# Optimization experiments

Hardware: AMD Instinct MI355X
Metric: run time of the kernel (lower is better)

The kernel has to match this reference:

```python
import jax, jax.numpy as jnp
import numpy as np

K = 3
K2 = K * K
EPS = 1e-5


def conv2d(x, w, stride=1, pad=1):
    return jax.lax.conv_general_dilated(
        x, w, (stride, stride), [(pad, pad), (pad, pad)],
        dimension_numbers=("NCHW", "OIHW", "NCHW"))


def bilinear_sample(x, py, px):
    """x: [B,C,H,W]; py,px: [B,Ho,Wo,K2] float sample coords.
    Zero padding outside bounds (torchvision deform_conv2d semantics).
    Returns [B,C,Ho,Wo,K2]."""
    B, C, H, W = x.shape
    Ho, Wo = py.shape[1], py.shape[2]
    y0 = jnp.floor(py)
    x0 = jnp.floor(px)
    wy1 = py - y0
    wx1 = px - x0
    x_flat = x.reshape(B, C, H * W)

    def gather(yi, xi):
        valid = (yi >= 0) & (yi < H) & (xi >= 0) & (xi < W)
        yc = jnp.clip(yi, 0, H - 1).astype(jnp.int32)
        xc = jnp.clip(xi, 0, W - 1).astype(jnp.int32)
        idx = (yc * W + xc).reshape(B, 1, -1)          # [B,1,N]
        v = jnp.take_along_axis(x_flat, idx, axis=2)   # [B,C,N]
        return v * valid.reshape(B, 1, -1).astype(x.dtype)

    w00 = ((1 - wy1) * (1 - wx1)).reshape(B, 1, -1)
    w01 = ((1 - wy1) * wx1).reshape(B, 1, -1)
    w10 = (wy1 * (1 - wx1)).reshape(B, 1, -1)
    w11 = (wy1 * wx1).reshape(B, 1, -1)
    val = (w00 * gather(y0, x0) + w01 * gather(y0, x0 + 1)
           + w10 * gather(y0 + 1, x0) + w11 * gather(y0 + 1, x0 + 1))
    return val.reshape(B, C, Ho, Wo, K2)


def deform_conv_bn_relu(x, d, offset_w, conv_w, gamma, beta):
    # offset branch: 3x3 conv on d, clamp to [-1,1]
    offset = jnp.clip(conv2d(d, offset_w, 1, 1), -1.0, 1.0)  # [B,2*K2,H,W]
    B, Cin, H, W = x.shape
    Cout = conv_w.shape[0]
    off = offset.reshape(B, K2, 2, H, W)
    dy = off[:, :, 0].transpose(0, 2, 3, 1)  # [B,H,W,K2]
    dx = off[:, :, 1].transpose(0, 2, 3, 1)
    kh = (jnp.arange(K2) // K).astype(jnp.float32)
    kw = (jnp.arange(K2) % K).astype(jnp.float32)
    # sample coords: out pixel + kernel tap - padding + learned offset
    py = (jnp.arange(H, dtype=jnp.float32)[None, :, None, None] - 1.0
          + kh[None, None, None, :] + dy)
    px = (jnp.arange(W, dtype=jnp.float32)[None, None, :, None] - 1.0
          + kw[None, None, None, :] + dx)
    sampled = bilinear_sample(x, py, px)  # [B,Cin,H,W,K2]
    out = jnp.einsum('bchwk,ock->bohw', sampled,
                     conv_w.reshape(Cout, Cin, K2))
    # BatchNorm2d (training forward: biased batch stats) + ReLU
    mean = out.mean(axis=(0, 2, 3))
    var = out.var(axis=(0, 2, 3))
    inv = gamma / jnp.sqrt(var + EPS)
    out = (out - mean[None, :, None, None]) * inv[None, :, None, None] \
        + beta[None, :, None, None]
    out = jax.nn.relu(out)
    return out, offset


def setup_inputs() -> dict:
    key = jax.random.key(0)
    k1, k2, k3, k4 = jax.random.split(key, 4)
    B, C, H, W = 4, 64, 160, 160
    Cout, offC = 64, 64
    x = jax.random.normal(k1, (B, C, H, W), dtype=jnp.float32)
    d = jax.random.normal(k2, (B, offC, H, W), dtype=jnp.float32)
    # torch zero-inits offset_conv; use small random weights so the
    # bilinear gather path is actually exercised with fractional offsets
    offset_w = jax.random.normal(k3, (2 * K2, offC, K, K), dtype=jnp.float32) * 0.01
    conv_w = jax.random.normal(k4, (Cout, C, K, K), dtype=jnp.float32) * (1.0 / np.sqrt(C * K2))
    gamma = jnp.ones((Cout,), dtype=jnp.float32)
    beta = jnp.zeros((Cout,), dtype=jnp.float32)
    return {"x": x, "d": d, "offset_w": offset_w, "conv_w": conv_w,
            "gamma": gamma, "beta": beta}


def reference(x, d, offset_w, conv_w, gamma, beta):
    return deform_conv_bn_relu(x, d, offset_w, conv_w, gamma, beta)
```

## Files before the change

### kernel.cpp

```cpp
#include <hip/hip_runtime.h>
#include <hip/hip_bf16.h>
#include <hip/hip_fp16.h>

#define BB 4
#define HH 160
#define WW 160
#define HWD (HH * WW)
#define OUT_ELEMS (BB * 64 * HWD)
#define EPSBN 1e-5f
#define CHSTRIDE (8 * HWD)
#define NSLOT 256

typedef _Float16 f16x8 __attribute__((ext_vector_type(8)));
typedef __attribute__((ext_vector_type(4))) float f32x4;

__device__ inline unsigned short f16bits(float a) {
  _Float16 h = (_Float16)a;
  unsigned short u;
  __builtin_memcpy(&u, &h, 2);
  return u;
}
__device__ inline unsigned packh2(float a, float b) {
  return (unsigned)f16bits(a) | ((unsigned)f16bits(b) << 16);
}

__device__ inline void tile_map(int blk, int& b, int& ty0, int& tx0) {
  int t = (blk & 7) * 200 + (blk >> 3);
  b = t / 400;
  int r = t % 400;
  ty0 = (r / 10) * 4;
  tx0 = (r % 10) * 16;
}

__global__ void prep_kernel(const float* __restrict__ cw,
                            const float* __restrict__ ow,
                            unsigned short* __restrict__ Bp,
                            unsigned short* __restrict__ B2p,
                            float* __restrict__ part) {
  int i = blockIdx.x * 256 + threadIdx.x;
  if (i < 32768) part[i] = 0.f;
  if (i < 49152) {
    int j = i & 7, l = (i >> 3) & 63, rest = i >> 9;
    int ki = rest % 24, nt = rest / 24;
    int kp = ki * 32 + ((l >> 4) << 3) + j;
    int chunk = kp / 96, kq = kp % 96;
    int t = kq >> 3, c = kq & 7;
    int n = nt * 16 + (l & 15);
    float v = (t < 9) ? cw[n * 576 + (chunk * 8 + c) * 9 + t] : 0.f;
    Bp[i] = f16bits(v);
  }
  if (i < 24576) {
    int j = i & 7, l = (i >> 3) & 63, rest = i >> 9;
    int ki = rest % 24, nt = rest / 24;
    int kp = ki * 32 + ((l >> 4) << 3) + j;
    int chunk = kp / 96, kq = kp % 96;
    int t = kq >> 3, c = kq & 7;
    int n = nt * 16 + (l & 15);
    float v = (t < 9 && n < 18) ? ow[n * 576 + (chunk * 8 + c) * 9 + t] : 0.f;
    B2p[i] = f16bits(v);
  }
}

__global__ __launch_bounds__(256) void fused_kernel(
    const float* __restrict__ x, const float* __restrict__ d,
    const f16x8* __restrict__ Bp, const f16x8* __restrict__ B2p,
    float* __restrict__ out, float* __restrict__ off_out,
    float* __restrict__ part) {
  int b, ty0, tx0;
  tile_map(blockIdx.x, b, ty0, tx0);
  const int tid = threadIdx.x;
  const int wv = tid >> 6, lane = tid & 63;
  const int lo = lane >> 4, li = lane & 15;

  __shared__ __align__(16) unsigned patch2[756];
  __shared__ f16x8 Af[768];
  __shared__ float offbuf[64 * 19];

  int gdo[2], gdl[2];
  bool gdk[2];
#pragma unroll
  for (int i = 0; i < 2; ++i) {
    int l = tid + i * 256;
    int p = l % 108, c2 = l / 108;
    int r = p / 18, col = p % 18;
    int gy = ty0 - 1 + r, gx = tx0 - 1 + col;
    gdk[i] = (l < 432) && gy >= 0 && gy < HH && gx >= 0 && gx < WW;
    gdo[i] = ((b * 64 + 2 * c2) * HH + gy) * WW + gx;
    gdl[i] = p * 4 + c2;
  }
  unsigned gd[2];
#pragma unroll
  for (int i = 0; i < 2; ++i)
    gd[i] = gdk[i] ? packh2(d[gdo[i]], d[gdo[i] + HWD]) : 0u;

  int gxo[3], gxl[3];
  bool gxk[3];
#pragma unroll
  for (int i = 0; i < 3; ++i) {
    int l = tid + i * 256;
    int p = l % 189, c2 = l / 189;
    int r = p / 21, col = p % 21;
    int gy = ty0 - 2 + r, gx2 = tx0 - 2 + col;
    gxk[i] = (l < 756) && gy >= 0 && gy < HH && gx2 >= 0 && gx2 < WW;
    gxo[i] = ((b * 64 + 2 * c2) * HH + gy) * WW + gx2;
    gxl[i] = p * 4 + c2;
  }
  unsigned gx[3];

  f32x4 acc0{0.f, 0.f, 0.f, 0.f}, acc1{0.f, 0.f, 0.f, 0.f};
  const int nt = wv >> 1, mh = wv & 1;
  int poffA[3];
#pragma unroll
  for (int kk = 0; kk < 3; ++kk) {
    int t = kk * 4 + lo;
    if (t > 8) t = 8;
    poffA[kk] = ((t / 3) * 18 + t % 3 + li) * 4;
  }

  for (int chunk = 0; chunk < 8; ++chunk) {
    f16x8 bw0 = B2p[((nt * 24 + chunk * 3 + 0) << 6) + lane];
    f16x8 bw1 = B2p[((nt * 24 + chunk * 3 + 1) << 6) + lane];
    f16x8 bw2 = B2p[((nt * 24 + chunk * 3 + 2) << 6) + lane];
#pragma unroll
    for (int i = 0; i < 2; ++i)
      if (tid + i * 256 < 432) patch2[gdl[i]] = gd[i];
    __syncthreads();
    if (chunk < 7) {
      int nco = (chunk + 1) * CHSTRIDE;
#pragma unroll
      for (int i = 0; i < 2; ++i)
        gd[i] = gdk[i] ? packh2(d[gdo[i] + nco], d[gdo[i] + nco + HWD]) : 0u;
    } else {
#pragma unroll
      for (int i = 0; i < 3; ++i)
        gx[i] = gxk[i] ? packh2(x[gxo[i]], x[gxo[i] + HWD]) : 0u;
    }
#pragma unroll
    for (int kk = 0; kk < 3; ++kk) {
      f16x8 bw = (kk == 0) ? bw0 : (kk == 1) ? bw1 : bw2;
      const f16x8* a0 = (const f16x8*)(patch2 + poffA[kk] + (mh * 2) * 72);
      const f16x8* a1 = (const f16x8*)(patch2 + poffA[kk] + (mh * 2 + 1) * 72);
      acc0 = __builtin_amdgcn_mfma_f32_16x16x32_f16(*a0, bw, acc0, 0, 0, 0);
      acc1 = __builtin_amdgcn_mfma_f32_16x16x32_f16(*a1, bw, acc1, 0, 0, 0);
    }
    __syncthreads();
  }

  const int nA = nt * 16 + li;
  if (nA < 18) {
#pragma unroll
    for (int f = 0; f < 2; ++f) {
      int mf = mh * 2 + f;
      f32x4 a = f ? acc1 : acc0;
      float4 v;
      v.x = fminf(1.f, fmaxf(-1.f, a[0]));
      v.y = fminf(1.f, fmaxf(-1.f, a[1]));
      v.z = fminf(1.f, fmaxf(-1.f, a[2]));
      v.w = fminf(1.f, fmaxf(-1.f, a[3]));
      offbuf[(mf * 16 + lo * 4 + 0) * 19 + nA] = v.x;
      offbuf[(mf * 16 + lo * 4 + 1) * 19 + nA] = v.y;
      offbuf[(mf * 16 + lo * 4 + 2) * 19 + nA] = v.z;
      offbuf[(mf * 16 + lo * 4 + 3) * 19 + nA] = v.w;
      *(float4*)(off_out + ((b * 18 + nA) * HH + ty0 + mf) * WW + tx0 +
                 lo * 4) = v;
    }
  }
  __syncthreads();

  const int h = ty0 + wv, w = tx0 + li;
  const int m_pix = wv * 16 + li;
  int bs[3];
  bool tre[3];
  __half2 w00h[3], w01h[3], w10h[3], w11h[3];
#pragma unroll
  for (int kk = 0; kk < 3; ++kk) {
    int t = kk * 4 + lo;
    tre[kk] = (t < 9);
    if (tre[kk]) {
      float dy = offbuf[m_pix * 19 + 2 * t];
      float dx = offbuf[m_pix * 19 + 2 * t + 1];
      float pyf = (float)(h - 1 + t / 3) + dy;
      float pxf = (float)(w - 1 + t % 3) + dx;
      float y0 = floorf(pyf), x0 = floorf(pxf);
      float wy = pyf - y0, wx = pxf - x0;
      bs[kk] = (((int)y0 - (ty0 - 2)) * 21 + ((int)x0 - (tx0 - 2))) * 4;
      w00h[kk] = __float2half2_rn((1.f - wy) * (1.f - wx));
      w01h[kk] = __float2half2_rn((1.f - wy) * wx);
      w10h[kk] = __float2half2_rn(wy * (1.f - wx));
      w11h[kk] = __float2half2_rn(wy * wx);
    } else {
      bs[kk] = 0;
      w00h[kk] = w01h[kk] = w10h[kk] = w11h[kk] = __float2half2_rn(0.f);
    }
  }

  f32x4 acc[4];
#pragma unroll
  for (int i = 0; i < 4; ++i) acc[i] = f32x4{0.f, 0.f, 0.f, 0.f};

  union u4h { uint4 q; __half2 hh[4]; unsigned u[4]; f16x8 v; };

  for (int chunk = 0; chunk < 8; ++chunk) {
    f16x8 bw0 = Bp[((wv * 24 + chunk * 3 + 0) << 6) + lane];
    f16x8 bw1 = Bp[((wv * 24 + chunk * 3 + 1) << 6) + lane];
    f16x8 bw2 = Bp[((wv * 24 + chunk * 3 + 2) << 6) + lane];
#pragma unroll
    for (int i = 0; i < 3; ++i)
      if (tid + i * 256 < 756) patch2[gxl[i]] = gx[i];
    __syncthreads();
    if (chunk < 7) {
      int nco = (chunk + 1) * CHSTRIDE;
#pragma unroll
      for (int i = 0; i < 3; ++i)
        gx[i] = gxk[i] ? packh2(x[gxo[i] + nco], x[gxo[i] + nco + HWD]) : 0u;
    }
#pragma unroll
    for (int kk = 0; kk < 3; ++kk) {
      u4h a;
      if (tre[kk]) {
        u4h q00, q01, q10, q11;
        q00.q = *(const uint4*)(patch2 + bs[kk]);
        q01.q = *(const uint4*)(patch2 + bs[kk] + 4);
        q10.q = *(const uint4*)(patch2 + bs[kk] + 84);
        q11.q = *(const uint4*)(patch2 + bs[kk] + 88);
#pragma unroll
        for (int j = 0; j < 4; ++j) {
          __half2 v = __hmul2(w00h[kk], q00.hh[j]);
          v = __hfma2(w01h[kk], q01.hh[j], v);
          v = __hfma2(w10h[kk], q10.hh[j], v);
          v = __hfma2(w11h[kk], q11.hh[j], v);
          a.hh[j] = v;
        }
      } else {
        a.u[0] = a.u[1] = a.u[2] = a.u[3] = 0u;
      }
      Af[((wv * 3 + kk) << 6) + lane] = a.v;
    }
    __syncthreads();
#pragma unroll
    for (int kk = 0; kk < 3; ++kk) {
      f16x8 bw = (kk == 0) ? bw0 : (kk == 1) ? bw1 : bw2;
#pragma unroll
      for (int mf = 0; mf < 4; ++mf)
        acc[mf] = __builtin_amdgcn_mfma_f32_16x16x32_f16(
            Af[((mf * 3 + kk) << 6) + lane], bw, acc[mf], 0, 0, 0);
    }
  }

  const int n = wv * 16 + li;
  float s = 0.f, s2 = 0.f;
#pragma unroll
  for (int mf = 0; mf < 4; ++mf) {
    float* po = out + ((b * 64 + n) * HH + ty0 + mf) * WW + tx0 + lo * 4;
    *(float4*)po = make_float4(acc[mf][0], acc[mf][1], acc[mf][2], acc[mf][3]);
#pragma unroll
    for (int r = 0; r < 4; ++r) {
      float v = acc[mf][r];
      s += v;
      s2 = fmaf(v, v, s2);
    }
  }
  s += __shfl_xor(s, 16);
  s += __shfl_xor(s, 32);
  s2 += __shfl_xor(s2, 16);
  s2 += __shfl_xor(s2, 32);
  if (lo == 0) {
    int slot = blockIdx.x & (NSLOT - 1);
    atomicAdd(&part[n * NSLOT + slot], s);
    atomicAdd(&part[(64 + n) * NSLOT + slot], s2);
  }
}

__global__ __launch_bounds__(256) void reduce_kernel(
    const float* __restrict__ part, double* __restrict__ sums) {
  const int j = blockIdx.x;
  __shared__ double sh[256];
  sh[threadIdx.x] = (double)part[j * NSLOT + threadIdx.x];
  __syncthreads();
  for (int t = 128; t > 0; t >>= 1) {
    if (threadIdx.x < t) sh[threadIdx.x] += sh[threadIdx.x + t];
    __syncthreads();
  }
  if (threadIdx.x == 0) sums[j] = sh[0];
}

__global__ __launch_bounds__(256) void bnapply_kernel(
    float* __restrict__ out, const double* __restrict__ sums,
    const float* __restrict__ gamma, const float* __restrict__ beta) {
  const int i = blockIdx.x * 256 + threadIdx.x;
  if (i >= OUT_ELEMS / 4) return;
  const int o = (i / (HWD / 4)) & 63;
  const float n_inv = 1.0f / (float)(BB * HWD);
  float mean = (float)sums[o] * n_inv;
  float var = (float)sums[64 + o] * n_inv - mean * mean;
  float inv = gamma[o] * rsqrtf(var + EPSBN);
  float bt = beta[o];
  float4 v = ((float4*)out)[i];
  v.x = fmaxf(0.f, (v.x - mean) * inv + bt);
  v.y = fmaxf(0.f, (v.y - mean) * inv + bt);
  v.z = fmaxf(0.f, (v.z - mean) * inv + bt);
  v.w = fmaxf(0.f, (v.w - mean) * inv + bt);
  ((float4*)out)[i] = v;
}

extern "C" void kernel_launch(void* const* d_in, const int* in_sizes, int n_in,
                              void* d_out, int out_size, void* d_ws, size_t ws_size,
                              hipStream_t stream) {
  const float* x = (const float*)d_in[0];
  const float* d = (const float*)d_in[1];
  const float* ow = (const float*)d_in[2];
  const float* cw = (const float*)d_in[3];
  const float* gamma = (const float*)d_in[4];
  const float* beta = (const float*)d_in[5];

  float* out = (float*)d_out;
  float* off_out = out + OUT_ELEMS;

  double* sums = (double*)d_ws;
  unsigned short* Bp = (unsigned short*)((char*)d_ws + 1024);
  unsigned short* B2p = Bp + 49152;
  float* part = (float*)(B2p + 24576);

  prep_kernel<<<192, 256, 0, stream>>>(cw, ow, Bp, B2p, part);

  fused_kernel<<<1600, 256, 0, stream>>>(
      x, d, (const f16x8*)Bp, (const f16x8*)B2p, out, off_out, part);

  reduce_kernel<<<128, 256, 0, stream>>>(part, sums);
  bnapply_kernel<<<(OUT_ELEMS / 4 + 255) / 256, 256, 0, stream>>>(
      out, sums, gamma, beta);
}
```

Baseline: 178.3 us.

## Fold BN stat reduction into apply kernel and linearize patch staging layout

Removes the separate reduce kernel: each block of the BN apply kernel now re-reduces the 256 partial slots for its channel with wave shuffles and a small shared array, then normalizes. This drops one launch and the double-precision reduction, at the cost of every block re-reading 2KB of partials and accumulating in float. It also changes the global-to-LDS staging index mapping so consecutive threads handle the four channel pairs of one pixel. That makes LDS stores linear and removes the modulo/divide address setup, though global reads for the patch are now strided across channels.

```diff
diff --git a/kernel.cpp b/kernel.cpp
--- a/kernel.cpp
+++ b/kernel.cpp
@@ -1,5 +1,4 @@
 #include <hip/hip_runtime.h>
-#include <hip/hip_bf16.h>
 #include <hip/hip_fp16.h>
 
 #define BB 4
@@ -74,36 +73,34 @@
 
   __shared__ __align__(16) unsigned patch2[756];
   __shared__ f16x8 Af[768];
-  __shared__ float offbuf[64 * 19];
-
-  int gdo[2], gdl[2];
+  __shared__ __align__(16) float offbuf[64 * 19];
+
+  int gdo[2];
   bool gdk[2];
 #pragma unroll
   for (int i = 0; i < 2; ++i) {
     int l = tid + i * 256;
-    int p = l % 108, c2 = l / 108;
+    int p = l >> 2, c2 = l & 3;
     int r = p / 18, col = p % 18;
     int gy = ty0 - 1 + r, gx = tx0 - 1 + col;
     gdk[i] = (l < 432) && gy >= 0 && gy < HH && gx >= 0 && gx < WW;
     gdo[i] = ((b * 64 + 2 * c2) * HH + gy) * WW + gx;
-    gdl[i] = p * 4 + c2;
   }
   unsigned gd[2];
 #pragma unroll
   for (int i = 0; i < 2; ++i)
     gd[i] = gdk[i] ? packh2(d[gdo[i]], d[gdo[i] + HWD]) : 0u;
 
-  int gxo[3], gxl[3];
+  int gxo[3];
   bool gxk[3];
 #pragma unroll
   for (int i = 0; i < 3; ++i) {
     int l = tid + i * 256;
-    int p = l % 189, c2 = l / 189;
+    int p = l >> 2, c2 = l & 3;
     int r = p / 21, col = p % 21;
     int gy = ty0 - 2 + r, gx2 = tx0 - 2 + col;
     gxk[i] = (l < 756) && gy >= 0 && gy < HH && gx2 >= 0 && gx2 < WW;
     gxo[i] = ((b * 64 + 2 * c2) * HH + gy) * WW + gx2;
-    gxl[i] = p * 4 + c2;
   }
   unsigned gx[3];
 
@@ -122,8 +119,10 @@
     f16x8 bw1 = B2p[((nt * 24 + chunk * 3 + 1) << 6) + lane];
     f16x8 bw2 = B2p[((nt * 24 + chunk * 3 + 2) << 6) + lane];
 #pragma unroll
-    for (int i = 0; i < 2; ++i)
-      if (tid + i * 256 < 432) patch2[gdl[i]] = gd[i];
+    for (int i = 0; i < 2; ++i) {
+      int l = tid + i * 256;
+      if (l < 432) patch2[l] = gd[i];
+    }
     __syncthreads();
     if (chunk < 7) {
       int nco = (chunk + 1) * CHSTRIDE;
@@ -205,8 +204,10 @@
     f16x8 bw1 = Bp[((wv * 24 + chunk * 3 + 1) << 6) + lane];
     f16x8 bw2 = Bp[((wv * 24 + chunk * 3 + 2) << 6) + lane];
 #pragma unroll
-    for (int i = 0; i < 3; ++i)
-      if (tid + i * 256 < 756) patch2[gxl[i]] = gx[i];
+    for (int i = 0; i < 3; ++i) {
+      int l = tid + i * 256;
+      if (l < 756) patch2[l] = gx[i];
+    }
     __syncthreads();
     if (chunk < 7) {
       int nco = (chunk + 1) * CHSTRIDE;
@@ -271,28 +272,29 @@
   }
 }
 
-__global__ __launch_bounds__(256) void reduce_kernel(
-    const float* __restrict__ part, double* __restrict__ sums) {
-  const int j = blockIdx.x;
-  __shared__ double sh[256];
-  sh[threadIdx.x] = (double)part[j * NSLOT + threadIdx.x];
-  __syncthreads();
-  for (int t = 128; t > 0; t >>= 1) {
-    if (threadIdx.x < t) sh[threadIdx.x] += sh[threadIdx.x + t];
-    __syncthreads();
-  }
-  if (threadIdx.x == 0) sums[j] = sh[0];
-}
-
-__global__ __launch_bounds__(256) void bnapply_kernel(
-    float* __restrict__ out, const double* __restrict__ sums,
+__global__ __launch_bounds__(256) void bn_final_kernel(
+    float* __restrict__ out, const float* __restrict__ part,
     const float* __restrict__ gamma, const float* __restrict__ beta) {
   const int i = blockIdx.x * 256 + threadIdx.x;
-  if (i >= OUT_ELEMS / 4) return;
   const int o = (i / (HWD / 4)) & 63;
+  const int tid = threadIdx.x, wv = tid >> 6;
+
+  float s = part[o * NSLOT + tid];
+  float s2 = part[(64 + o) * NSLOT + tid];
+#pragma unroll
+  for (int sh = 1; sh < 64; sh <<= 1) {
+    s += __shfl_xor(s, sh);
+    s2 += __shfl_xor(s2, sh);
+  }
+  __shared__ float red[8];
+  if ((tid & 63) == 0) { red[wv] = s; red[4 + wv] = s2; }
+  __syncthreads();
+  s = red[0] + red[1] + red[2] + red[3];
+  s2 = red[4] + red[5] + red[6] + red[7];
+
   const float n_inv = 1.0f / (float)(BB * HWD);
-  float mean = (float)sums[o] * n_inv;
-  float var = (float)sums[64 + o] * n_inv - mean * mean;
+  float mean = s * n_inv;
+  float var = s2 * n_inv - mean * mean;
   float inv = gamma[o] * rsqrtf(var + EPSBN);
   float bt = beta[o];
   float4 v = ((float4*)out)[i];
@@ -316,8 +318,7 @@
   float* out = (float*)d_out;
   float* off_out = out + OUT_ELEMS;
 
-  double* sums = (double*)d_ws;
-  unsigned short* Bp = (unsigned short*)((char*)d_ws + 1024);
+  unsigned short* Bp = (unsigned short*)d_ws;
   unsigned short* B2p = Bp + 49152;
   float* part = (float*)(B2p + 24576);
 
@@ -326,7 +327,6 @@
   fused_kernel<<<1600, 256, 0, stream>>>(
       x, d, (const f16x8*)Bp, (const f16x8*)B2p, out, off_out, part);
 
-  reduce_kernel<<<128, 256, 0, stream>>>(part, sums);
-  bnapply_kernel<<<(OUT_ELEMS / 4 + 255) / 256, 256, 0, stream>>>(
-      out, sums, gamma, beta);
-}
+  bn_final_kernel<<<OUT_ELEMS / 4 / 256, 256, 0, stream>>>(
+      out, part, gamma, beta);
+}
```

New measurement: 173.9 us. -2.4%, faster.
